# Optimization experiments

Hardware: AMD Instinct MI355X
Metric: run time of the kernel (lower is better)

Reference implementation:

```python
import jax, jax.numpy as jnp
import numpy as np
from jax import lax

NSAMPLE = 1024
SEM_NUM = 20


def weighted_fps(xyz, w, nsample):
    # xyz: [B,N,3], w: [B,N] -> idx [B,nsample] int32
    # Iterative weighted furthest point sampling: start at index 0, keep the
    # min squared distance to the selected set, pick argmax(min_dist * weight).
    B, N, _ = xyz.shape
    barange = jnp.arange(B)

    def step(carry, _):
        min_d, last = carry                      # [B,N], [B]
        lp = xyz[barange, last]                  # [B,3] last selected points
        d = jnp.sum((xyz - lp[:, None, :]) ** 2, axis=-1)  # [B,N]
        min_d = jnp.minimum(min_d, d)
        nxt = jnp.argmax(min_d * w, axis=1).astype(jnp.int32)
        return (min_d, nxt), nxt

    init = (jnp.full((B, N), 1e10, xyz.dtype), jnp.zeros((B,), jnp.int32))
    _, rest = lax.scan(step, init, None, length=nsample - 1)   # [nsample-1, B]
    idx = jnp.concatenate([jnp.zeros((1, B), jnp.int32), rest], axis=0)
    return idx.T                                               # [B, nsample]


def setup_inputs() -> dict:
    key = jax.random.key(0)
    k1, k2, k3 = jax.random.split(key, 3)
    B, N, C = 16, 16384, 128
    xyz = jax.random.normal(k1, (B, N, 3), dtype=jnp.float32)
    seg_feature = jax.random.normal(k2, (B, C, N), dtype=jnp.float32)
    seg_label = jax.random.randint(k3, (B, N), 0, SEM_NUM, dtype=jnp.int32)
    return {"xyz": xyz, "seg_feature": seg_feature, "seg_label": seg_label}


def reference(xyz, seg_feature, seg_label):
    # class frequency weights: count[b,c] = #points of class c in cloud b
    counts = jnp.sum(jax.nn.one_hot(seg_label, SEM_NUM, dtype=jnp.float32), axis=1)  # [B,SEM]
    seg_weights = jnp.take_along_axis(counts, seg_label, axis=1)                     # [B,N]
    idx = weighted_fps(lax.stop_gradient(xyz), seg_weights, NSAMPLE)                 # [B,S]
    sampled_xyz = jnp.take_along_axis(xyz, idx[:, :, None], axis=1)                  # [B,S,3]
    sample_seg_feature = jnp.take_along_axis(seg_feature, idx[:, None, :], axis=2)   # [B,C,S]
    sample_seg_label = jnp.take_along_axis(seg_label, idx, axis=1)                   # [B,S]
    return sampled_xyz, sample_seg_feature, sample_seg_label
```

## Files before the change

### kernel.cpp

```cpp
#include <hip/hip_runtime.h>


#define FPS_B   16
#define FPS_N   16384
#define FPS_C   128
#define FPS_S   1024
#define FPS_SEM 20
#define FPS_T   1024
#define FPS_PPT 16

typedef unsigned long long ull;

template <int CTRL>
__device__ __forceinline__ float dpp_movf(float v) {
  return __uint_as_float(__builtin_amdgcn_update_dpp(
      __float_as_uint(v), __float_as_uint(v), CTRL, 0xF, 0xF, true));
}

__global__ __launch_bounds__(FPS_T)
__attribute__((amdgpu_waves_per_eu(4, 4)))
void wfps_kernel(
    const float* __restrict__ xyz,
    const int*   __restrict__ label,
    int*         __restrict__ idx_out)
{
  const int b = blockIdx.x;
  const int t = threadIdx.x;
  const int lane = t & 63;

  __shared__ int counts[FPS_SEM];
  __shared__ unsigned wmax32[FPS_S];
  __shared__ int widx[FPS_S];

  if (t < FPS_SEM) counts[t] = 0;
  wmax32[t] = 0u;
  widx[t] = 0x7FFFFFFF;
  __syncthreads();

  const int* lab = label + b * FPS_N;
  int mylab[FPS_PPT];
#pragma unroll
  for (int k = 0; k < FPS_PPT; ++k) {
    mylab[k] = lab[t + k * FPS_T];
    atomicAdd(&counts[mylab[k]], 1);
  }
  __syncthreads();

  const float* xb = xyz + b * FPS_N * 3;
  float px[FPS_PPT], py[FPS_PPT], pz[FPS_PPT], w[FPS_PPT], mind[FPS_PPT];
#pragma unroll
  for (int k = 0; k < FPS_PPT; ++k) {
    int n = t + k * FPS_T;
    px[k] = xb[n * 3 + 0];
    py[k] = xb[n * 3 + 1];
    pz[k] = xb[n * 3 + 2];
    w[k] = (float)counts[mylab[k]];
    mind[k] = 1e10f;
    asm("" : "+v"(px[k]), "+v"(py[k]), "+v"(pz[k]), "+v"(w[k]));
  }

  if (t == 0) idx_out[b * FPS_S] = 0;
  float lx = xb[0], ly = xb[1], lz = xb[2];

  for (int s = 1; s < FPS_S; ++s) {
    float bs = -1.0f;
    int bk = 0;
#pragma unroll
    for (int k = 0; k < FPS_PPT; ++k) {
      float dx = __fsub_rn(px[k], lx);
      float dy = __fsub_rn(py[k], ly);
      float dz = __fsub_rn(pz[k], lz);
      float d  = __fadd_rn(__fadd_rn(__fmul_rn(dx, dx), __fmul_rn(dy, dy)),
                           __fmul_rn(dz, dz));
      float m = fminf(mind[k], d);
      mind[k] = m;
      float sc = __fmul_rn(m, w[k]);
      bool g = sc > bs;
      bs = g ? sc : bs;
      bk = g ? k : bk;
    }

    float m = bs;
    m = fmaxf(m, dpp_movf<0xB1>(m));
    m = fmaxf(m, dpp_movf<0x4E>(m));
    m = fmaxf(m, dpp_movf<0x141>(m));
    m = fmaxf(m, dpp_movf<0x140>(m));
    m = fmaxf(m, __shfl_xor(m, 16, 64));
    m = fmaxf(m, __shfl_xor(m, 32, 64));

    if (lane == 0) atomicMax(&wmax32[s], __float_as_uint(m));
    __syncthreads();

    unsigned M = wmax32[s];
    if (__float_as_uint(bs) == M)
      atomicMin(&widx[s], t + (bk << 10));
    __syncthreads();

    int cur = widx[s];
    if (t == 0) idx_out[b * FPS_S + s] = cur;

    const float* q = xb + 3 * cur;
    lx = q[0]; ly = q[1]; lz = q[2];
  }
}

__global__ void gather_kernel(
    const float* __restrict__ xyz,
    const float* __restrict__ feat,
    const int*   __restrict__ label,
    const int*   __restrict__ idx,
    float*       __restrict__ out)
{
  const long long FEAT = (long long)FPS_B * FPS_C * FPS_S;
  const int XYZN = FPS_B * FPS_S * 3;
  const int LABN = FPS_B * FPS_S;
  long long i = (long long)blockIdx.x * blockDim.x + threadIdx.x;

  if (i < FEAT) {
    int s = (int)(i & (FPS_S - 1));
    int c = (int)((i >> 10) & (FPS_C - 1));
    int b = (int)(i >> 17);
    int n = idx[b * FPS_S + s];
    out[XYZN + i] = feat[((long long)(b * FPS_C + c)) * FPS_N + n];
  } else if (i < FEAT + XYZN) {
    int j = (int)(i - FEAT);
    int d = j % 3;
    int sb = j / 3;
    int s = sb & (FPS_S - 1);
    int b = sb >> 10;
    int n = idx[b * FPS_S + s];
    out[j] = xyz[((long long)b * FPS_N + n) * 3 + d];
  } else if (i < FEAT + XYZN + LABN) {
    int j = (int)(i - FEAT - XYZN);
    int s = j & (FPS_S - 1);
    int b = j >> 10;
    int n = idx[b * FPS_S + s];
    out[FEAT + XYZN + j] = (float)label[b * FPS_N + n];
  }
}

extern "C" void kernel_launch(void* const* d_in, const int* in_sizes, int n_in,
                              void* d_out, int out_size, void* d_ws, size_t ws_size,
                              hipStream_t stream) {
  const float* xyz   = (const float*)d_in[0];
  const float* feat  = (const float*)d_in[1];
  const int*   label = (const int*)d_in[2];
  float* out = (float*)d_out;
  int*   idx = (int*)d_ws;

  wfps_kernel<<<FPS_B, FPS_T, 0, stream>>>(xyz, label, idx);

  const long long total = (long long)FPS_B * FPS_C * FPS_S
                        + (long long)FPS_B * FPS_S * 3
                        + (long long)FPS_B * FPS_S;
  gather_kernel<<<(int)((total + 255) / 256), 256, 0, stream>>>(
      xyz, feat, label, idx, out);
}
```

Baseline: 1.639 ms.

## Move half of per-thread point coordinates from registers into LDS

```diff
diff --git a/kernel.cpp b/kernel.cpp
--- a/kernel.cpp
+++ b/kernel.cpp
@@ -8,6 +8,8 @@
 #define FPS_SEM 20
 #define FPS_T   1024
 #define FPS_PPT 16
+#define FPS_KR  8
+#define FPS_KL  8
 
 typedef unsigned long long ull;
 
@@ -29,6 +31,7 @@
   const int lane = t & 63;
 
   __shared__ int counts[FPS_SEM];
+  __shared__ float4 pts[FPS_KL][FPS_T];
   __shared__ unsigned wmax32[FPS_S];
   __shared__ int widx[FPS_S];
 
@@ -47,26 +50,42 @@
   __syncthreads();
 
   const float* xb = xyz + b * FPS_N * 3;
-  float px[FPS_PPT], py[FPS_PPT], pz[FPS_PPT], w[FPS_PPT], mind[FPS_PPT];
+
 #pragma unroll
-  for (int k = 0; k < FPS_PPT; ++k) {
+  for (int k = 0; k < FPS_KL; ++k) {
+    int n = t + (k + FPS_KR) * FPS_T;
+    float4 p;
+    p.x = xb[n * 3 + 0];
+    p.y = xb[n * 3 + 1];
+    p.z = xb[n * 3 + 2];
+    p.w = (float)counts[mylab[k + FPS_KR]];
+    pts[k][t] = p;
+  }
+
+  float px[FPS_KR], py[FPS_KR], pz[FPS_KR], w[FPS_KR];
+#pragma unroll
+  for (int k = 0; k < FPS_KR; ++k) {
     int n = t + k * FPS_T;
     px[k] = xb[n * 3 + 0];
     py[k] = xb[n * 3 + 1];
     pz[k] = xb[n * 3 + 2];
     w[k] = (float)counts[mylab[k]];
-    mind[k] = 1e10f;
     asm("" : "+v"(px[k]), "+v"(py[k]), "+v"(pz[k]), "+v"(w[k]));
   }
 
+  float mind[FPS_PPT];
+#pragma unroll
+  for (int k = 0; k < FPS_PPT; ++k) mind[k] = 1e10f;
+
   if (t == 0) idx_out[b * FPS_S] = 0;
   float lx = xb[0], ly = xb[1], lz = xb[2];
+  __syncthreads();
 
   for (int s = 1; s < FPS_S; ++s) {
     float bs = -1.0f;
     int bk = 0;
 #pragma unroll
-    for (int k = 0; k < FPS_PPT; ++k) {
+    for (int k = 0; k < FPS_KR; ++k) {
       float dx = __fsub_rn(px[k], lx);
       float dy = __fsub_rn(py[k], ly);
       float dz = __fsub_rn(pz[k], lz);
@@ -78,6 +97,21 @@
       bool g = sc > bs;
       bs = g ? sc : bs;
       bk = g ? k : bk;
+    }
+#pragma unroll
+    for (int k = 0; k < FPS_KL; ++k) {
+      float4 p = pts[k][t];
+      float dx = __fsub_rn(p.x, lx);
+      float dy = __fsub_rn(p.y, ly);
+      float dz = __fsub_rn(p.z, lz);
+      float d  = __fadd_rn(__fadd_rn(__fmul_rn(dx, dx), __fmul_rn(dy, dy)),
+                           __fmul_rn(dz, dz));
+      float m = fminf(mind[k + FPS_KR], d);
+      mind[k + FPS_KR] = m;
+      float sc = __fmul_rn(m, p.w);
+      bool g = sc > bs;
+      bs = g ? sc : bs;
+      bk = g ? (k + FPS_KR) : bk;
     }
 
     float m = bs;
@@ -96,7 +130,7 @@
       atomicMin(&widx[s], t + (bk << 10));
     __syncthreads();
 
-    int cur = widx[s];
+    int cur = __builtin_amdgcn_readfirstlane(widx[s]);
     if (t == 0) idx_out[b * FPS_S + s] = cur;
 
     const float* q = xb + 3 * cur;
```

Result: slower. 1.778 ms (+8.5%).
